# Optimization experiments

Hardware: AMD Instinct MI355X
Metric: run time of the kernel (lower is better)

## Reference

```python
import jax, jax.numpy as jnp
import numpy as np
import math

D_MODEL = 1024
N_HEAD = 16
D_HEAD = D_MODEL // N_HEAD
SCALE = math.sqrt(D_HEAD)
B, S = 8, 512


def setup_inputs() -> dict:
    key = jax.random.key(0)
    ks = jax.random.split(key, 7)
    x = jax.random.normal(ks[0], (B, S, D_MODEL), dtype=jnp.float32)
    mask = jnp.ones((B, S), dtype=jnp.int32)
    qmask = jax.random.randint(ks[1], (B, S), 0, 2).astype(jnp.int32)
    # params
    Wqkv = jax.random.normal(ks[2], (4 * D_MODEL, D_MODEL), dtype=jnp.float32) / math.sqrt(D_MODEL)
    fc_w = jax.random.normal(ks[3], (D_MODEL, D_MODEL), dtype=jnp.float32) / math.sqrt(D_MODEL)
    fc_b = jnp.zeros((D_MODEL,), dtype=jnp.float32)
    shift = jnp.abs(jax.random.normal(ks[4], (1,), dtype=jnp.float32)) + 0.001
    bias = -jnp.abs(jax.random.normal(ks[5], (1,), dtype=jnp.float32))
    return {"x": x, "mask": mask, "qmask": qmask, "Wqkv": Wqkv,
            "fc_w": fc_w, "fc_b": fc_b, "shift": shift, "bias": bias}


def reference(x, mask, qmask, Wqkv, fc_w, fc_b, shift, bias):
    Bsz, L, D = x.shape
    qkv = x @ Wqkv.T  # [B,S,4D], no bias
    q, k1, k2, v = jnp.split(qkv, 4, axis=-1)

    def heads(t):  # [B,S,D] -> [B,H,S,dh]
        return t.reshape(Bsz, L, N_HEAD, D_HEAD).transpose(0, 2, 1, 3)

    q, k1, k2, v = heads(q), heads(k1), heads(k2), heads(v)

    attn_self = jnp.einsum('bhqd,bhkd->bhqk', q, k1)
    attn_others = jnp.einsum('bhqd,bhkd->bhqk', q, k2)
    same_spk = (qmask[:, :, None] == qmask[:, None, :])[:, None]  # [B,1,S,S]
    attn = jnp.where(same_spk, attn_self, attn_others) / SCALE

    # key padding mask
    attn = jnp.where((mask == 0)[:, None, None, :], -jnp.inf, attn)

    # Gaussian distance bias: -(shift*(i-j)^2 + bias)
    pos = jnp.arange(L, dtype=jnp.float32)
    sq_dist = (pos[:, None] - pos[None, :]) ** 2  # [S,S]
    attn = attn - (shift[0] * sq_dist + bias[0])

    p = jax.nn.softmax(attn, axis=-1)  # dropout=0 (eval)
    out = jnp.einsum('bhqk,bhkd->bhqd', p, v)
    out = out.transpose(0, 2, 1, 3).reshape(Bsz, L, D)
    return out @ fc_w.T + fc_b
```

## Files before the change

kernel.cpp:

```cpp
#include <hip/hip_runtime.h>

typedef unsigned short u16;
typedef __bf16 bf16_t;
typedef bf16_t bf16x8 __attribute__((ext_vector_type(8)));
typedef float f32x4 __attribute__((ext_vector_type(4)));
typedef u16 u16x8 __attribute__((ext_vector_type(8)));
typedef u16 u16x4 __attribute__((ext_vector_type(4)));

__device__ __forceinline__ u16 f2b(float f) {
    unsigned int u = __float_as_uint(f);
    u += 0x7fffu + ((u >> 16) & 1u);
    return (u16)(u >> 16);
}

__device__ __forceinline__ f32x4 mfma16(u16x8 a, u16x8 b, f32x4 c) {
    return __builtin_amdgcn_mfma_f32_16x16x32_bf16(
        __builtin_bit_cast(bf16x8, a), __builtin_bit_cast(bf16x8, b), c, 0, 0, 0);
}

#define GLDS16(gp, lp)                                                          \
    __builtin_amdgcn_global_load_lds(                                           \
        (const __attribute__((address_space(1))) void*)(gp),                    \
        (__attribute__((address_space(3))) void*)(lp), 16, 0, 0)

__global__ __launch_bounds__(256) void cvt3_kernel(const float* __restrict__ s0,
                                                   const float* __restrict__ s1,
                                                   const float* __restrict__ s2,
                                                   u16* __restrict__ d0,
                                                   u16* __restrict__ d1,
                                                   u16* __restrict__ d2) {
    int i = (blockIdx.x * 256 + threadIdx.x) * 4;
    const float* src; u16* dst;
    if (i < 4194304)       { src = s0;           dst = d0;           }
    else if (i < 8388608)  { src = s1 - 4194304; dst = d1 - 4194304; }
    else                   { src = s2 - 8388608; dst = d2 - 8388608; }
    float4 f = *(const float4*)(src + i);
    u16x4 o = { f2b(f.x), f2b(f.y), f2b(f.z), f2b(f.w) };
    *(u16x4*)(dst + i) = o;
}

__global__ __launch_bounds__(512, 2) void gemm256_qkv(
    const u16* __restrict__ A, const u16* __restrict__ Bw,
    u16* __restrict__ Qf, u16* __restrict__ K1f,
    u16* __restrict__ K2f, u16* __restrict__ Vf)
{
    __shared__ u16 lds[4][2][8192];

    const int t = threadIdx.x;
    const int lane = t & 63;
    const int w = t >> 6;
    const int wm = w >> 2, wn = w & 3;
    const int lr = lane & 15, quad = lane >> 4;

    const int lin = blockIdx.x;
    const int swz = (lin & 7) * 32 + (lin >> 3);
    const int bx = swz & 15, by = swz >> 4;
    const int tileM = by * 256, tileN = bx * 256;

    const int srow = t >> 2;
    const int scol = ((t & 3) ^ ((t >> 3) & 3)) * 8;
    const u16* Asrc0 = A + (size_t)(tileM + srow) * 1024 + scol;
    const u16* Asrc1 = Asrc0 + (size_t)128 * 1024;
    const u16* Bsrc0 = Bw + (size_t)(tileN + srow) * 1024 + scol;
    const u16* Bsrc1 = Bsrc0 + (size_t)128 * 1024;

    const int swzq = (quad ^ ((lr >> 1) & 3)) * 8;
    const int aoff = (wm * 128 + lr) * 32 + swzq;
    const int boff = (wn * 64 + lr) * 32 + swzq;

    f32x4 acc[8][4] = {};

#define STAGE_A(tk, buf)                                                        \
    do { GLDS16(Asrc0 + (tk) * 32, &lds[buf][0][t * 8]);                        \
         GLDS16(Asrc1 + (tk) * 32, &lds[buf][0][(t + 512) * 8]); } while (0)
#define STAGE_B(tk, buf)                                                        \
    do { GLDS16(Bsrc0 + (tk) * 32, &lds[buf][1][t * 8]);                        \
         GLDS16(Bsrc1 + (tk) * 32, &lds[buf][1][(t + 512) * 8]); } while (0)

#define DO_TILE(tk, DO_ST, VMASM)                                               \
    do {                                                                        \
        const int cur_ = (tk) & 3, nxt_ = ((tk) + 3) & 3;                       \
        const u16* aL = &lds[cur_][0][0];                                       \
        const u16* bL = &lds[cur_][1][0];                                       \
        if (DO_ST) { STAGE_A((tk) + 3, nxt_); STAGE_B((tk) + 3, nxt_); }        \
        u16x8 af[8], bf[4];                                                     \
        _Pragma("unroll") for (int i = 0; i < 4; ++i)                           \
            bf[i] = *(const u16x8*)(bL + boff + i * 512);                       \
        _Pragma("unroll") for (int i = 0; i < 8; ++i)                           \
            af[i] = *(const u16x8*)(aL + aoff + i * 512);                       \
        __builtin_amdgcn_s_setprio(1);                                          \
        _Pragma("unroll") for (int mi = 0; mi < 8; ++mi)                        \
            _Pragma("unroll") for (int ni = 0; ni < 4; ++ni)                    \
                acc[mi][ni] = mfma16(af[mi], bf[ni], acc[mi][ni]);              \
        __builtin_amdgcn_s_setprio(0);                                          \
        VMASM;                                                                  \
        __builtin_amdgcn_s_barrier();                                           \
    } while (0)

    STAGE_A(0, 0); STAGE_B(0, 0);
    STAGE_A(1, 1); STAGE_B(1, 1);
    STAGE_A(2, 2); STAGE_B(2, 2);
    asm volatile("s_waitcnt vmcnt(8)" ::: "memory");
    __builtin_amdgcn_s_barrier();

#pragma unroll 4
    for (int tk = 0; tk < 28; ++tk)
        DO_TILE(tk, true, asm volatile("s_waitcnt vmcnt(8)" ::: "memory"));
    DO_TILE(28, true,  asm volatile("s_waitcnt vmcnt(8)" ::: "memory"));
    DO_TILE(29, false, asm volatile("s_waitcnt vmcnt(4)" ::: "memory"));
    DO_TILE(30, false, asm volatile("s_waitcnt vmcnt(0)" ::: "memory"));
    DO_TILE(31, false, (void)0);
#undef DO_TILE
#undef STAGE_A
#undef STAGE_B

    const int kv = tileN >> 10;
    const int h  = ((tileN + wn * 64) >> 6) & 15;
    const int bh = (((tileM + wm * 128) >> 9) << 4) + h;
    const int M16 = ((tileM & 511) + wm * 128) >> 4;
    const int M32 = M16 >> 1;

    if (kv < 3) {
        u16* base = (kv == 0) ? Qf : (kv == 1) ? K1f : K2f;
#pragma unroll
        for (int mi = 0; mi < 8; ++mi)
#pragma unroll
            for (int ni = 0; ni < 4; ++ni) {
                size_t idx0 = ((size_t)((bh * 32 + M16 + mi) * 2 + (ni >> 1))) * 512
                            + (((ni * 2 + (lr >> 3)) & 3) * 16 + quad * 4) * 8 + (lr & 7);
#pragma unroll
                for (int r = 0; r < 4; ++r)
                    base[idx0 + r * 8] = f2b(acc[mi][ni][r]);
            }
    } else {
#pragma unroll
        for (int mi = 0; mi < 8; ++mi)
#pragma unroll
            for (int ni = 0; ni < 4; ++ni) {
                size_t idx = ((size_t)((bh * 4 + ni) * 16 + M32 + (mi >> 1))) * 512
                           + (((mi * 2 + (quad >> 1)) & 3) * 16 + lr) * 8 + (quad & 1) * 4;
                u16x4 o = { f2b(acc[mi][ni][0]), f2b(acc[mi][ni][1]),
                            f2b(acc[mi][ni][2]), f2b(acc[mi][ni][3]) };
                *(u16x4*)(Vf + idx) = o;
            }
    }
}

template <int MT, int MODE>
__global__ __launch_bounds__(256) void gemm_bt(
    const u16* __restrict__ A, const u16* __restrict__ Bw,
    u16* __restrict__ Qf, u16* __restrict__ K1f,
    u16* __restrict__ K2f, u16* __restrict__ Vf,
    float* __restrict__ Cf, const float* __restrict__ biasp)
{
    constexpr int K = 1024;
    constexpr int MF = MT / 32;
    __shared__ u16 As[2][MT * 32];
    __shared__ u16 Bs[2][128 * 32];
    const int t = threadIdx.x;
    const int lane = t & 63;
    const int w = t >> 6;
    const int wm = w >> 1, wn = w & 1;
    const int lr = lane & 15, quad = lane >> 4;
    const int tileM = blockIdx.y * MT, tileN = blockIdx.x * 128;

    f32x4 acc[MF][4] = {};

    const u16* Ag = A + (size_t)(tileM + (t >> 2)) * K + (t & 3) * 8;
    const u16* Bg = Bw + (size_t)(tileN + (t >> 2)) * K + (t & 3) * 8;

#define STAGE(kk, bufi)                                                         \
    do {                                                                        \
        GLDS16(Ag + (kk), &As[bufi][t * 8]);                                    \
        if (MT == 128) GLDS16(Ag + (kk) + 64 * K, &As[bufi][t * 8 + 2048]);     \
        GLDS16(Bg + (kk), &Bs[bufi][t * 8]);                                    \
        GLDS16(Bg + (kk) + 64 * K, &Bs[bufi][t * 8 + 2048]);                    \
    } while (0)

    STAGE(0, 0);
    __syncthreads();

#pragma unroll 2
    for (int kk = 0; kk < K; kk += 32) {
        const int cur = (kk >> 5) & 1;
        if (kk + 32 < K) STAGE(kk + 32, cur ^ 1);

        u16x8 af[MF], bf[4];
#pragma unroll
        for (int i = 0; i < MF; ++i)
            af[i] = *(const u16x8*)(&As[cur][(wm * (MT / 2) + i * 16 + lr) * 32 + quad * 8]);
#pragma unroll
        for (int i = 0; i < 4; ++i)
            bf[i] = *(const u16x8*)(&Bs[cur][(wn * 64 + i * 16 + lr) * 32 + quad * 8]);
#pragma unroll
        for (int mi = 0; mi < MF; ++mi)
#pragma unroll
            for (int ni = 0; ni < 4; ++ni)
                acc[mi][ni] = mfma16(af[mi], bf[ni], acc[mi][ni]);

        __syncthreads();
    }
#undef STAGE

    if (MODE == 0) {
#pragma unroll
        for (int mi = 0; mi < MF; ++mi)
#pragma unroll
            for (int ni = 0; ni < 4; ++ni) {
                int n = tileN + wn * 64 + ni * 16 + lr;
                int kv = n >> 10;
                int h = (n >> 6) & 15, d = n & 63;
#pragma unroll
                for (int r = 0; r < 4; ++r) {
                    int m = tileM + wm * (MT / 2) + mi * 16 + quad * 4 + r;
                    int s = m & 511, bh = ((m >> 9) << 4) + h;
                    u16 v = f2b(acc[mi][ni][r]);
                    if (kv < 3) {
                        u16* base = (kv == 0) ? Qf : (kv == 1) ? K1f : K2f;
                        size_t idx = ((size_t)((bh * 32 + (s >> 4)) * 2 + (d >> 5))) * 512
                                   + (((d >> 3) & 3) * 16 + (s & 15)) * 8 + (d & 7);
                        base[idx] = v;
                    } else {
                        size_t idx = ((size_t)((bh * 4 + (d >> 4)) * 16 + (s >> 5))) * 512
                                   + (((s >> 3) & 3) * 16 + (d & 15)) * 8 + (s & 7);
                        Vf[idx] = v;
                    }
                }
            }
    } else {
#pragma unroll
        for (int mi = 0; mi < MF; ++mi)
#pragma unroll
            for (int ni = 0; ni < 4; ++ni) {
                int n = tileN + wn * 64 + ni * 16 + lr;
                float bv = biasp[n];
#pragma unroll
                for (int r = 0; r < 4; ++r) {
                    int m = tileM + wm * (MT / 2) + mi * 16 + quad * 4 + r;
                    Cf[(size_t)m * 1024 + n] = acc[mi][ni][r] + bv;
                }
            }
    }
}

__global__ __launch_bounds__(256, 2) void attn_kernel(
    const u16* __restrict__ qfm, const u16* __restrict__ k1fm,
    const u16* __restrict__ k2fm, const u16* __restrict__ vfm,
    const int* __restrict__ maskp, const int* __restrict__ qmaskp,
    const float* __restrict__ shiftp, const float* __restrict__ biasp,
    u16* __restrict__ ao)
{
    __shared__ u16 Ks[2][2][2][2][512];
    __shared__ u16 Vs[2][4][512];
    __shared__ u16 Pw[4][2][512];

    const int bh = blockIdx.x & 127, qh = blockIdx.x >> 7;
    const int b = bh >> 4;
    const int t = threadIdx.x, lane = t & 63, w = t >> 6;
    const int lr = lane & 15, quad = lane >> 4;
    const float shiftv = shiftp[0], biasv = biasp[0];

    const int m16a = qh * 8 + w;
    const int m16b = m16a + 4;
    const int qbaseA = m16a * 16;
    const int qbaseB = m16b * 16;

    const u16* qsrcA = qfm + ((size_t)(bh * 32 + m16a) * 2) * 512 + lane * 8;
    const u16* qsrcB = qfm + ((size_t)(bh * 32 + m16b) * 2) * 512 + lane * 8;
    u16x8 qa0 = *(const u16x8*)(qsrcA);
    u16x8 qa1 = *(const u16x8*)(qsrcA + 512);
    u16x8 qb0 = *(const u16x8*)(qsrcB);
    u16x8 qb1 = *(const u16x8*)(qsrcB + 512);

    int qmrA[4], qmrB[4]; float rowfA[4], rowfB[4];
#pragma unroll
    for (int r = 0; r < 4; ++r) {
        int ma = qbaseA + quad * 4 + r;
        int mb = qbaseB + quad * 4 + r;
        qmrA[r] = qmaskp[b * 512 + ma];
        qmrB[r] = qmaskp[b * 512 + mb];
        rowfA[r] = (float)ma;
        rowfB[r] = (float)mb;
    }

    f32x4 oa0 = {0,0,0,0}, oa1 = {0,0,0,0}, oa2 = {0,0,0,0}, oa3 = {0,0,0,0};
    f32x4 ob0 = {0,0,0,0}, ob1 = {0,0,0,0}, ob2 = {0,0,0,0}, ob3 = {0,0,0,0};
    float lsa[4] = {0,0,0,0}, lsb[4] = {0,0,0,0};

    u16* pbA = &Pw[w][0][0];
    u16* pbB = &Pw[w][1][0];
    const int wa0 = quad * 128 + (((lr >> 3) ^ quad) * 8) + (lr & 7);
    const int wa1 = quad * 128 + (((2 | (lr >> 3)) ^ quad) * 8) + (lr & 7);
    const int ra = lr * 32 + ((quad ^ (lr >> 2)) * 8);

    const int s_ = w >> 1, kh_ = w & 1;
    const u16* k1s = k1fm + ((size_t)(bh * 32 + s_) * 2 + kh_) * 512 + lane * 8;
    const u16* k2s = k2fm + ((size_t)(bh * 32 + s_) * 2 + kh_) * 512 + lane * 8;
    const u16* vsrc = vfm + ((size_t)(bh * 4 + w) * 16) * 512 + lane * 8;

#define ASTAGE(cc, bufi)                                                        \
    do {                                                                        \
        GLDS16(k1s + (size_t)(cc) * 2048, &Ks[bufi][0][s_][kh_][lane * 8]);     \
        GLDS16(k2s + (size_t)(cc) * 2048, &Ks[bufi][1][s_][kh_][lane * 8]);     \
        GLDS16(vsrc + (size_t)(cc) * 512, &Vs[bufi][w][lane * 8]);              \
    } while (0)

    const int* qmb = qmaskp + b * 512;
    const int* kmb = maskp + b * 512;

    ASTAGE(0, 0);
    __syncthreads();

    for (int cc = 0; cc < 16; ++cc) {
        const int cur = cc & 1;
        if (cc < 15) ASTAGE(cc + 1, cur ^ 1);

        u16x8 k1t0a = *(const u16x8*)(&Ks[cur][0][0][0][lane * 8]);
        u16x8 k1t0b = *(const u16x8*)(&Ks[cur][0][0][1][lane * 8]);
        u16x8 k1t1a = *(const u16x8*)(&Ks[cur][0][1][0][lane * 8]);
        u16x8 k1t1b = *(const u16x8*)(&Ks[cur][0][1][1][lane * 8]);
        u16x8 k2t0a = *(const u16x8*)(&Ks[cur][1][0][0][lane * 8]);
        u16x8 k2t0b = *(const u16x8*)(&Ks[cur][1][0][1][lane * 8]);
        u16x8 k2t1a = *(const u16x8*)(&Ks[cur][1][1][0][lane * 8]);
        u16x8 k2t1b = *(const u16x8*)(&Ks[cur][1][1][1][lane * 8]);

        f32x4 z = {0.f, 0.f, 0.f, 0.f};
        f32x4 sa1t0 = mfma16(qa1, k1t0b, mfma16(qa0, k1t0a, z));
        f32x4 sa2t0 = mfma16(qa1, k2t0b, mfma16(qa0, k2t0a, z));
        f32x4 sa1t1 = mfma16(qa1, k1t1b, mfma16(qa0, k1t1a, z));
        f32x4 sa2t1 = mfma16(qa1, k2t1b, mfma16(qa0, k2t1a, z));
        f32x4 sb1t0 = mfma16(qb1, k1t0b, mfma16(qb0, k1t0a, z));
        f32x4 sb2t0 = mfma16(qb1, k2t0b, mfma16(qb0, k2t0a, z));
        f32x4 sb1t1 = mfma16(qb1, k1t1b, mfma16(qb0, k1t1a, z));
        f32x4 sb2t1 = mfma16(qb1, k2t1b, mfma16(qb0, k2t1a, z));

        const int col0 = cc * 32 + lr, col1 = col0 + 16;
        const int qmc0 = qmb[col0], qmc1 = qmb[col1];
        const float ka0 = (kmb[col0] ? 0.f : -1e30f) - 10.0f;
        const float ka1 = (kmb[col1] ? 0.f : -1e30f) - 10.0f;
        const float colf0 = (float)col0, colf1 = (float)col1;

        u16x8 vf0 = *(const u16x8*)(&Vs[cur][0][lane * 8]);
        u16x8 vf1 = *(const u16x8*)(&Vs[cur][1][lane * 8]);
        u16x8 vf2 = *(const u16x8*)(&Vs[cur][2][lane * 8]);
        u16x8 vf3 = *(const u16x8*)(&Vs[cur][3][lane * 8]);

        {
            float p0[4], p1[4];
#pragma unroll
            for (int r = 0; r < 4; ++r) {
                float d0 = rowfA[r] - colf0;
                float d1 = rowfA[r] - colf1;
                float sel0 = (qmrA[r] == qmc0) ? sa1t0[r] : sa2t0[r];
                float sel1 = (qmrA[r] == qmc1) ? sa1t1[r] : sa2t1[r];
                float v0 = fmaf(sel0, 0.125f, -fmaf(shiftv * d0, d0, biasv)) + ka0;
                float v1 = fmaf(sel1, 0.125f, -fmaf(shiftv * d1, d1, biasv)) + ka1;
                p0[r] = __expf(v0);
                p1[r] = __expf(v1);
                lsa[r] += p0[r] + p1[r];
            }
#pragma unroll
            for (int r = 0; r < 4; ++r) {
                pbA[wa0 + r * 32] = f2b(p0[r]);
                pbA[wa1 + r * 32] = f2b(p1[r]);
            }
            u16x8 af = *(const u16x8*)(pbA + ra);
            oa0 = mfma16(af, vf0, oa0);
            oa1 = mfma16(af, vf1, oa1);
            oa2 = mfma16(af, vf2, oa2);
            oa3 = mfma16(af, vf3, oa3);
        }
        {
            float p0[4], p1[4];
#pragma unroll
            for (int r = 0; r < 4; ++r) {
                float d0 = rowfB[r] - colf0;
                float d1 = rowfB[r] - colf1;
                float sel0 = (qmrB[r] == qmc0) ? sb1t0[r] : sb2t0[r];
                float sel1 = (qmrB[r] == qmc1) ? sb1t1[r] : sb2t1[r];
                float v0 = fmaf(sel0, 0.125f, -fmaf(shiftv * d0, d0, biasv)) + ka0;
                float v1 = fmaf(sel1, 0.125f, -fmaf(shiftv * d1, d1, biasv)) + ka1;
                p0[r] = __expf(v0);
                p1[r] = __expf(v1);
                lsb[r] += p0[r] + p1[r];
            }
#pragma unroll
            for (int r = 0; r < 4; ++r) {
                pbB[wa0 + r * 32] = f2b(p0[r]);
                pbB[wa1 + r * 32] = f2b(p1[r]);
            }
            u16x8 af = *(const u16x8*)(pbB + ra);
            ob0 = mfma16(af, vf0, ob0);
            ob1 = mfma16(af, vf1, ob1);
            ob2 = mfma16(af, vf2, ob2);
            ob3 = mfma16(af, vf3, ob3);
        }

        __syncthreads();
    }
#undef ASTAGE

#pragma unroll
    for (int r = 0; r < 4; ++r) {
        float s = lsa[r];
#pragma unroll
        for (int m = 1; m < 16; m <<= 1) s += __shfl_xor(s, m);
        float inv = 1.0f / s;
        int grow = b * 512 + qbaseA + quad * 4 + r;
        u16* orow = ao + (size_t)grow * 1024 + (bh & 15) * 64 + lr;
        orow[0]  = f2b(oa0[r] * inv);
        orow[16] = f2b(oa1[r] * inv);
        orow[32] = f2b(oa2[r] * inv);
        orow[48] = f2b(oa3[r] * inv);
    }
#pragma unroll
    for (int r = 0; r < 4; ++r) {
        float s = lsb[r];
#pragma unroll
        for (int m = 1; m < 16; m <<= 1) s += __shfl_xor(s, m);
        float inv = 1.0f / s;
        int grow = b * 512 + qbaseB + quad * 4 + r;
        u16* orow = ao + (size_t)grow * 1024 + (bh & 15) * 64 + lr;
        orow[0]  = f2b(ob0[r] * inv);
        orow[16] = f2b(ob1[r] * inv);
        orow[32] = f2b(ob2[r] * inv);
        orow[48] = f2b(ob3[r] * inv);
    }
}

extern "C" void kernel_launch(void* const* d_in, const int* in_sizes, int n_in,
                              void* d_out, int out_size, void* d_ws, size_t ws_size,
                              hipStream_t stream) {
    (void)in_sizes; (void)n_in; (void)out_size; (void)ws_size;
    const float* x      = (const float*)d_in[0];
    const int*   maskp  = (const int*)d_in[1];
    const int*   qmaskp = (const int*)d_in[2];
    const float* Wqkv   = (const float*)d_in[3];
    const float* fc_w   = (const float*)d_in[4];
    const float* fc_b   = (const float*)d_in[5];
    const float* shiftp = (const float*)d_in[6];
    const float* biasp  = (const float*)d_in[7];
    float* out = (float*)d_out;

    char* ws = (char*)d_ws;
    u16* xb   = (u16*)(ws);
    u16* wb   = (u16*)(ws + (8u << 20));
    u16* fwb  = (u16*)(ws + (16u << 20));
    u16* qfm  = (u16*)(ws + (18u << 20));
    u16* k1fm = (u16*)(ws + (26u << 20));
    u16* k2fm = (u16*)(ws + (34u << 20));
    u16* vfm  = (u16*)(ws + (42u << 20));
    u16* aob  = (u16*)(ws + (50u << 20));

    cvt3_kernel<<<9216, 256, 0, stream>>>(x, Wqkv, fc_w, xb, wb, fwb);
    gemm256_qkv<<<256, 512, 0, stream>>>(xb, wb, qfm, k1fm, k2fm, vfm);
    attn_kernel<<<512, 256, 0, stream>>>(qfm, k1fm, k2fm, vfm, maskp, qmaskp,
                                         shiftp, biasp, aob);
    gemm_bt<64, 1><<<dim3(8, 64), 256, 0, stream>>>(aob, fwb, nullptr, nullptr,
                                                    nullptr, nullptr, out, fc_b);
}
```

Baseline: 185.4 us.

## Shrink QKV GEMM tile to 128x128 with XCD-aware block mapping

```diff
diff --git a/kernel.cpp b/kernel.cpp
--- a/kernel.cpp
+++ b/kernel.cpp
@@ -39,43 +39,43 @@
     *(u16x4*)(dst + i) = o;
 }
 
-__global__ __launch_bounds__(512, 2) void gemm256_qkv(
+__global__ __launch_bounds__(256, 2) void gemm128_qkv(
     const u16* __restrict__ A, const u16* __restrict__ Bw,
     u16* __restrict__ Qf, u16* __restrict__ K1f,
     u16* __restrict__ K2f, u16* __restrict__ Vf)
 {
-    __shared__ u16 lds[4][2][8192];
+    __shared__ u16 lds[4][2][4096];
 
     const int t = threadIdx.x;
     const int lane = t & 63;
     const int w = t >> 6;
-    const int wm = w >> 2, wn = w & 3;
+    const int wm = w >> 1, wn = w & 1;
     const int lr = lane & 15, quad = lane >> 4;
 
     const int lin = blockIdx.x;
-    const int swz = (lin & 7) * 32 + (lin >> 3);
-    const int bx = swz & 15, by = swz >> 4;
-    const int tileM = by * 256, tileN = bx * 256;
-
-    const int srow = t >> 2;
+    const int xcd = lin & 7, j = lin >> 3;
+    const int bx = (xcd & 1) * 16 + (j & 15);
+    const int by = (xcd >> 1) * 8 + (j >> 4);
+    const int tileM = by * 128, tileN = bx * 128;
+
     const int scol = ((t & 3) ^ ((t >> 3) & 3)) * 8;
-    const u16* Asrc0 = A + (size_t)(tileM + srow) * 1024 + scol;
-    const u16* Asrc1 = Asrc0 + (size_t)128 * 1024;
-    const u16* Bsrc0 = Bw + (size_t)(tileN + srow) * 1024 + scol;
-    const u16* Bsrc1 = Bsrc0 + (size_t)128 * 1024;
+    const u16* Asrc0 = A + (size_t)(tileM + (t >> 2)) * 1024 + scol;
+    const u16* Asrc1 = Asrc0 + (size_t)64 * 1024;
+    const u16* Bsrc0 = Bw + (size_t)(tileN + (t >> 2)) * 1024 + scol;
+    const u16* Bsrc1 = Bsrc0 + (size_t)64 * 1024;
 
     const int swzq = (quad ^ ((lr >> 1) & 3)) * 8;
-    const int aoff = (wm * 128 + lr) * 32 + swzq;
+    const int aoff = (wm * 64 + lr) * 32 + swzq;
     const int boff = (wn * 64 + lr) * 32 + swzq;
 
-    f32x4 acc[8][4] = {};
+    f32x4 acc[4][4] = {};
 
 #define STAGE_A(tk, buf)                                                        \
     do { GLDS16(Asrc0 + (tk) * 32, &lds[buf][0][t * 8]);                        \
-         GLDS16(Asrc1 + (tk) * 32, &lds[buf][0][(t + 512) * 8]); } while (0)
+         GLDS16(Asrc1 + (tk) * 32, &lds[buf][0][(t + 256) * 8]); } while (0)
 #define STAGE_B(tk, buf)                                                        \
     do { GLDS16(Bsrc0 + (tk) * 32, &lds[buf][1][t * 8]);                        \
-         GLDS16(Bsrc1 + (tk) * 32, &lds[buf][1][(t + 512) * 8]); } while (0)
+         GLDS16(Bsrc1 + (tk) * 32, &lds[buf][1][(t + 256) * 8]); } while (0)
 
 #define DO_TILE(tk, DO_ST, VMASM)                                               \
     do {                                                                        \
@@ -83,13 +83,13 @@
         const u16* aL = &lds[cur_][0][0];                                       \
         const u16* bL = &lds[cur_][1][0];                                       \
         if (DO_ST) { STAGE_A((tk) + 3, nxt_); STAGE_B((tk) + 3, nxt_); }        \
-        u16x8 af[8], bf[4];                                                     \
+        u16x8 af[4], bf[4];                                                     \
+        _Pragma("unroll") for (int i = 0; i < 4; ++i)                           \
+            af[i] = *(const u16x8*)(aL + aoff + i * 512);                       \
         _Pragma("unroll") for (int i = 0; i < 4; ++i)                           \
             bf[i] = *(const u16x8*)(bL + boff + i * 512);                       \
-        _Pragma("unroll") for (int i = 0; i < 8; ++i)                           \
-            af[i] = *(const u16x8*)(aL + aoff + i * 512);                       \
         __builtin_amdgcn_s_setprio(1);                                          \
-        _Pragma("unroll") for (int mi = 0; mi < 8; ++mi)                        \
+        _Pragma("unroll") for (int mi = 0; mi < 4; ++mi)                        \
             _Pragma("unroll") for (int ni = 0; ni < 4; ++ni)                    \
                 acc[mi][ni] = mfma16(af[mi], bf[ni], acc[mi][ni]);              \
         __builtin_amdgcn_s_setprio(0);                                          \
@@ -114,36 +114,30 @@
 #undef STAGE_A
 #undef STAGE_B
 
-    const int kv = tileN >> 10;
-    const int h  = ((tileN + wn * 64) >> 6) & 15;
-    const int bh = (((tileM + wm * 128) >> 9) << 4) + h;
-    const int M16 = ((tileM & 511) + wm * 128) >> 4;
-    const int M32 = M16 >> 1;
-
-    if (kv < 3) {
-        u16* base = (kv == 0) ? Qf : (kv == 1) ? K1f : K2f;
-#pragma unroll
-        for (int mi = 0; mi < 8; ++mi)
-#pragma unroll
-            for (int ni = 0; ni < 4; ++ni) {
-                size_t idx0 = ((size_t)((bh * 32 + M16 + mi) * 2 + (ni >> 1))) * 512
-                            + (((ni * 2 + (lr >> 3)) & 3) * 16 + quad * 4) * 8 + (lr & 7);
-#pragma unroll
-                for (int r = 0; r < 4; ++r)
-                    base[idx0 + r * 8] = f2b(acc[mi][ni][r]);
-            }
-    } else {
-#pragma unroll
-        for (int mi = 0; mi < 8; ++mi)
-#pragma unroll
-            for (int ni = 0; ni < 4; ++ni) {
-                size_t idx = ((size_t)((bh * 4 + ni) * 16 + M32 + (mi >> 1))) * 512
-                           + (((mi * 2 + (quad >> 1)) & 3) * 16 + lr) * 8 + (quad & 1) * 4;
-                u16x4 o = { f2b(acc[mi][ni][0]), f2b(acc[mi][ni][1]),
-                            f2b(acc[mi][ni][2]), f2b(acc[mi][ni][3]) };
-                *(u16x4*)(Vf + idx) = o;
-            }
-    }
+#pragma unroll
+    for (int mi = 0; mi < 4; ++mi)
+#pragma unroll
+        for (int ni = 0; ni < 4; ++ni) {
+            int n = tileN + wn * 64 + ni * 16 + lr;
+            int kv = n >> 10;
+            int h = (n >> 6) & 15, d = n & 63;
+#pragma unroll
+            for (int r = 0; r < 4; ++r) {
+                int m = tileM + wm * 64 + mi * 16 + quad * 4 + r;
+                int s = m & 511, bh = ((m >> 9) << 4) + h;
+                u16 v = f2b(acc[mi][ni][r]);
+                if (kv < 3) {
+                    u16* base = (kv == 0) ? Qf : (kv == 1) ? K1f : K2f;
+                    size_t idx = ((size_t)((bh * 32 + (s >> 4)) * 2 + (d >> 5))) * 512
+                               + (((d >> 3) & 3) * 16 + (s & 15)) * 8 + (d & 7);
+                    base[idx] = v;
+                } else {
+                    size_t idx = ((size_t)((bh * 4 + (d >> 4)) * 16 + (s >> 5))) * 512
+                               + (((s >> 3) & 3) * 16 + (d & 15)) * 8 + (s & 7);
+                    Vf[idx] = v;
+                }
+            }
+        }
 }
 
 template <int MT, int MODE>
@@ -453,7 +447,7 @@
     u16* aob  = (u16*)(ws + (50u << 20));
 
     cvt3_kernel<<<9216, 256, 0, stream>>>(x, Wqkv, fc_w, xb, wb, fwb);
-    gemm256_qkv<<<256, 512, 0, stream>>>(xb, wb, qfm, k1fm, k2fm, vfm);
+    gemm128_qkv<<<1024, 256, 0, stream>>>(xb, wb, qfm, k1fm, k2fm, vfm);
     attn_kernel<<<512, 256, 0, stream>>>(qfm, k1fm, k2fm, vfm, maskp, qmaskp,
                                          shiftp, biasp, aob);
     gemm_bt<64, 1><<<dim3(8, 64), 256, 0, stream>>>(aob, fwb, nullptr, nullptr,
```

Measured after the change: 192.4 us. +3.8%, slower.

## Rewrite output projection GEMM with 128x128 tiles, 4-stage pipeline and swizzled LDS

Applied to the files above, without the earlier changes.

```diff
diff --git a/kernel.cpp b/kernel.cpp
--- a/kernel.cpp
+++ b/kernel.cpp
@@ -146,101 +146,92 @@
     }
 }
 
-template <int MT, int MODE>
-__global__ __launch_bounds__(256) void gemm_bt(
+__global__ __launch_bounds__(256, 2) void gemm128_proj(
     const u16* __restrict__ A, const u16* __restrict__ Bw,
-    u16* __restrict__ Qf, u16* __restrict__ K1f,
-    u16* __restrict__ K2f, u16* __restrict__ Vf,
     float* __restrict__ Cf, const float* __restrict__ biasp)
 {
-    constexpr int K = 1024;
-    constexpr int MF = MT / 32;
-    __shared__ u16 As[2][MT * 32];
-    __shared__ u16 Bs[2][128 * 32];
+    __shared__ u16 lds[4][2][4096];
+
     const int t = threadIdx.x;
     const int lane = t & 63;
     const int w = t >> 6;
     const int wm = w >> 1, wn = w & 1;
     const int lr = lane & 15, quad = lane >> 4;
-    const int tileM = blockIdx.y * MT, tileN = blockIdx.x * 128;
-
-    f32x4 acc[MF][4] = {};
-
-    const u16* Ag = A + (size_t)(tileM + (t >> 2)) * K + (t & 3) * 8;
-    const u16* Bg = Bw + (size_t)(tileN + (t >> 2)) * K + (t & 3) * 8;
-
-#define STAGE(kk, bufi)                                                         \
+
+    const int lin = blockIdx.x;
+    const int xcd = lin & 7, j = lin >> 3;
+    const int bx = j & 7;
+    const int by = xcd * 4 + (j >> 3);
+    const int tileM = by * 128, tileN = bx * 128;
+
+    const int scol = ((t & 3) ^ ((t >> 3) & 3)) * 8;
+    const u16* Asrc0 = A + (size_t)(tileM + (t >> 2)) * 1024 + scol;
+    const u16* Asrc1 = Asrc0 + (size_t)64 * 1024;
+    const u16* Bsrc0 = Bw + (size_t)(tileN + (t >> 2)) * 1024 + scol;
+    const u16* Bsrc1 = Bsrc0 + (size_t)64 * 1024;
+
+    const int swzq = (quad ^ ((lr >> 1) & 3)) * 8;
+    const int aoff = (wm * 64 + lr) * 32 + swzq;
+    const int boff = (wn * 64 + lr) * 32 + swzq;
+
+    f32x4 acc[4][4] = {};
+
+#define STAGE_A(tk, buf)                                                        \
+    do { GLDS16(Asrc0 + (tk) * 32, &lds[buf][0][t * 8]);                        \
+         GLDS16(Asrc1 + (tk) * 32, &lds[buf][0][(t + 256) * 8]); } while (0)
+#define STAGE_B(tk, buf)                                                        \
+    do { GLDS16(Bsrc0 + (tk) * 32, &lds[buf][1][t * 8]);                        \
+         GLDS16(Bsrc1 + (tk) * 32, &lds[buf][1][(t + 256) * 8]); } while (0)
+
+#define DO_TILE(tk, DO_ST, VMASM)                                               \
     do {                                                                        \
-        GLDS16(Ag + (kk), &As[bufi][t * 8]);                                    \
-        if (MT == 128) GLDS16(Ag + (kk) + 64 * K, &As[bufi][t * 8 + 2048]);     \
-        GLDS16(Bg + (kk), &Bs[bufi][t * 8]);                                    \
-        GLDS16(Bg + (kk) + 64 * K, &Bs[bufi][t * 8 + 2048]);                    \
+        const int cur_ = (tk) & 3, nxt_ = ((tk) + 3) & 3;                       \
+        const u16* aL = &lds[cur_][0][0];                                       \
+        const u16* bL = &lds[cur_][1][0];                                       \
+        if (DO_ST) { STAGE_A((tk) + 3, nxt_); STAGE_B((tk) + 3, nxt_); }        \
+        u16x8 af[4], bf[4];                                                     \
+        _Pragma("unroll") for (int i = 0; i < 4; ++i)                           \
+            af[i] = *(const u16x8*)(aL + aoff + i * 512);                       \
+        _Pragma("unroll") for (int i = 0; i < 4; ++i)                           \
+            bf[i] = *(const u16x8*)(bL + boff + i * 512);                       \
+        __builtin_amdgcn_s_setprio(1);                                          \
+        _Pragma("unroll") for (int mi = 0; mi < 4; ++mi)                        \
+            _Pragma("unroll") for (int ni = 0; ni < 4; ++ni)                    \
+                acc[mi][ni] = mfma16(af[mi], bf[ni], acc[mi][ni]);              \
+        __builtin_amdgcn_s_setprio(0);                                          \
+        VMASM;                                                                  \
+        __builtin_amdgcn_s_barrier();                                           \
     } while (0)
 
-    STAGE(0, 0);
-    __syncthreads();
-
-#pragma unroll 2
-    for (int kk = 0; kk < K; kk += 32) {
-        const int cur = (kk >> 5) & 1;
-        if (kk + 32 < K) STAGE(kk + 32, cur ^ 1);
-
-        u16x8 af[MF], bf[4];
-#pragma unroll
-        for (int i = 0; i < MF; ++i)
-            af[i] = *(const u16x8*)(&As[cur][(wm * (MT / 2) + i * 16 + lr) * 32 + quad * 8]);
-#pragma unroll
-        for (int i = 0; i < 4; ++i)
-            bf[i] = *(const u16x8*)(&Bs[cur][(wn * 64 + i * 16 + lr) * 32 + quad * 8]);
-#pragma unroll
-        for (int mi = 0; mi < MF; ++mi)
-#pragma unroll
-            for (int ni = 0; ni < 4; ++ni)
-                acc[mi][ni] = mfma16(af[mi], bf[ni], acc[mi][ni]);
-
-        __syncthreads();
-    }
-#undef STAGE
-
-    if (MODE == 0) {
-#pragma unroll
-        for (int mi = 0; mi < MF; ++mi)
-#pragma unroll
-            for (int ni = 0; ni < 4; ++ni) {
-                int n = tileN + wn * 64 + ni * 16 + lr;
-                int kv = n >> 10;
-                int h = (n >> 6) & 15, d = n & 63;
-#pragma unroll
-                for (int r = 0; r < 4; ++r) {
-                    int m = tileM + wm * (MT / 2) + mi * 16 + quad * 4 + r;
-                    int s = m & 511, bh = ((m >> 9) << 4) + h;
-                    u16 v = f2b(acc[mi][ni][r]);
-                    if (kv < 3) {
-                        u16* base = (kv == 0) ? Qf : (kv == 1) ? K1f : K2f;
-                        size_t idx = ((size_t)((bh * 32 + (s >> 4)) * 2 + (d >> 5))) * 512
-                                   + (((d >> 3) & 3) * 16 + (s & 15)) * 8 + (d & 7);
-                        base[idx] = v;
-                    } else {
-                        size_t idx = ((size_t)((bh * 4 + (d >> 4)) * 16 + (s >> 5))) * 512
-                                   + (((s >> 3) & 3) * 16 + (d & 15)) * 8 + (s & 7);
-                        Vf[idx] = v;
-                    }
-                }
-            }
-    } else {
-#pragma unroll
-        for (int mi = 0; mi < MF; ++mi)
-#pragma unroll
-            for (int ni = 0; ni < 4; ++ni) {
-                int n = tileN + wn * 64 + ni * 16 + lr;
-                float bv = biasp[n];
-#pragma unroll
-                for (int r = 0; r < 4; ++r) {
-                    int m = tileM + wm * (MT / 2) + mi * 16 + quad * 4 + r;
-                    Cf[(size_t)m * 1024 + n] = acc[mi][ni][r] + bv;
-                }
-            }
-    }
+    STAGE_A(0, 0); STAGE_B(0, 0);
+    STAGE_A(1, 1); STAGE_B(1, 1);
+    STAGE_A(2, 2); STAGE_B(2, 2);
+    asm volatile("s_waitcnt vmcnt(8)" ::: "memory");
+    __builtin_amdgcn_s_barrier();
+
+#pragma unroll 4
+    for (int tk = 0; tk < 28; ++tk)
+        DO_TILE(tk, true, asm volatile("s_waitcnt vmcnt(8)" ::: "memory"));
+    DO_TILE(28, true,  asm volatile("s_waitcnt vmcnt(8)" ::: "memory"));
+    DO_TILE(29, false, asm volatile("s_waitcnt vmcnt(4)" ::: "memory"));
+    DO_TILE(30, false, asm volatile("s_waitcnt vmcnt(0)" ::: "memory"));
+    DO_TILE(31, false, (void)0);
+#undef DO_TILE
+#undef STAGE_A
+#undef STAGE_B
+
+#pragma unroll
+    for (int mi = 0; mi < 4; ++mi)
+#pragma unroll
+        for (int ni = 0; ni < 4; ++ni) {
+            int n = tileN + wn * 64 + ni * 16 + lr;
+            float bv = biasp[n];
+#pragma unroll
+            for (int r = 0; r < 4; ++r) {
+                int m = tileM + wm * 64 + mi * 16 + quad * 4 + r;
+                Cf[(size_t)m * 1024 + n] = acc[mi][ni][r] + bv;
+            }
+        }
 }
 
 __global__ __launch_bounds__(256, 2) void attn_kernel(
@@ -456,6 +447,5 @@
     gemm256_qkv<<<256, 512, 0, stream>>>(xb, wb, qfm, k1fm, k2fm, vfm);
     attn_kernel<<<512, 256, 0, stream>>>(qfm, k1fm, k2fm, vfm, maskp, qmaskp,
                                          shiftp, biasp, aob);
-    gemm_bt<64, 1><<<dim3(8, 64), 256, 0, stream>>>(aob, fwb, nullptr, nullptr,
-                                                    nullptr, nullptr, out, fc_b);
-}
+    gemm128_proj<<<256, 256, 0, stream>>>(aob, fwb, out, fc_b);
+}
```

Result: faster. 175.2 us, median of 2 (-5.5%).
